# Kernel tuning notes

Hardware: AMD Instinct MI355X
Metric: run time of the kernel (lower is better)

The kernel has to match this reference:

```python
import jax, jax.numpy as jnp
from jax import lax
import numpy as np

H = 2048
LX = 32
LY = 32


def setup_inputs() -> dict:
    key = jax.random.key(0)
    ks = jax.random.split(key, 9)
    N = LX * LY
    s = 1.0 / np.sqrt(H).astype(np.float32)
    inp = {
        "x": jax.random.normal(ks[0], (N,), jnp.float32),
        # embed: Dense(1 -> H)
        "We": jax.random.normal(ks[1], (1, H), jnp.float32),
        "be": jnp.zeros((H,), jnp.float32),
        # GRUCell input gates (with bias)
        "Wir": jax.random.normal(ks[2], (H, H), jnp.float32) * s,
        "bir": jnp.zeros((H,), jnp.float32),
        "Wiz": jax.random.normal(ks[3], (H, H), jnp.float32) * s,
        "biz": jnp.zeros((H,), jnp.float32),
        "Win": jax.random.normal(ks[4], (H, H), jnp.float32) * s,
        "bin_": jnp.zeros((H,), jnp.float32),
        # GRUCell recurrent gates (hr/hz bias-free, hn with bias, as in flax)
        "Whr": jax.random.normal(ks[5], (H, H), jnp.float32) * s,
        "Whz": jax.random.normal(ks[6], (H, H), jnp.float32) * s,
        "Whn": jax.random.normal(ks[7], (H, H), jnp.float32) * s,
        "bhn": jnp.zeros((H,), jnp.float32),
        "Lx": LX,
        "Ly": LY,
    }
    return inp


def snake_order(Lx: int, Ly: int):
    idx = np.arange(Lx * Ly).reshape(Ly, Lx)
    idx[1::2] = idx[1::2, ::-1]  # reverse odd rows -> snake pattern
    return jnp.asarray(idx.reshape(-1))


def reference(x, We, be, Wir, bir, Wiz, biz, Win, bin_, Whr, Whz, Whn, bhn, Lx, Ly):
    order = snake_order(Lx, Ly)                      # (N,) visit order
    # embed each scalar site value: Dense(1->H), vectorized over all sites
    xe = x[order][:, None] * We[0][None, :] + be     # (N, H)
    # precompute input-gate projections for all steps (same math, batched)
    a_r = xe @ Wir + bir                             # (N, H)
    a_z = xe @ Wiz + biz
    a_n = xe @ Win + bin_
    h0 = jnp.zeros((Whr.shape[0],), xe.dtype)

    def step(h, g):
        ar, az, an = g
        r = jax.nn.sigmoid(ar + h @ Whr)
        z = jax.nn.sigmoid(az + h @ Whz)
        n = jnp.tanh(an + r * (h @ Whn + bhn))
        h_new = (1.0 - z) * n + z * h
        return h_new, None

    h, _ = lax.scan(step, h0, (a_r, a_z, a_n))
    return h
```

## Files before the change

kernel.cpp:

```cpp
#include <hip/hip_runtime.h>

#define HDIM 2048
#define TSTEPS 1024
#define NBLK 256
#define NTHR 512

typedef unsigned long long ull;

__device__ __forceinline__ int snake_src(int t) {
    int y = t >> 5, p = t & 31;
    return (y & 1) ? (y * 32 + 31 - p) : t;
}
__device__ __forceinline__ float sigmoid_f(float v) {
    return __builtin_amdgcn_rcpf(1.f + __expf(-v));
}
__device__ __forceinline__ float tanh_f(float v) {
    return 1.f - 2.f * __builtin_amdgcn_rcpf(__expf(2.f * v) + 1.f);
}

__global__ __launch_bounds__(NTHR, 2) void gru_all(
    const float* __restrict__ x,
    const float* __restrict__ We,  const float* __restrict__ be,
    const float* __restrict__ Wir, const float* __restrict__ bir,
    const float* __restrict__ Wiz, const float* __restrict__ biz,
    const float* __restrict__ Win, const float* __restrict__ bin_,
    const float* __restrict__ Whr, const float* __restrict__ Whz,
    const float* __restrict__ Whn, const float* __restrict__ bhn,
    float* __restrict__ out, ull* __restrict__ s0, ull* __restrict__ s1)
{
    const int tid  = threadIdx.x;
    const int blk  = blockIdx.x;
    const int c    = tid & 7;
    const int r    = tid >> 3;
    const int col  = blk * 8 + c;
    const int row0 = r * 32;
    const int lane = tid & 63, wv = tid >> 6;

    __shared__ __align__(16) float lds_h[2304];
    __shared__ float sBe[HDIM];
    __shared__ float red[8][6][8];

    for (int i = tid; i < HDIM; i += NTHR) { lds_h[i] = We[i]; sBe[i] = be[i]; }
    __syncthreads();

    float wr[32], wz[32], wn[32];
#pragma unroll
    for (int k = 0; k < 32; ++k) {
        size_t off = (size_t)(row0 + k) * HDIM + col;
        wr[k] = Whr[off];
        wz[k] = Whz[off];
        wn[k] = Whn[off];
    }

    float eR=0,eZ=0,eN=0,bRa=0,bZa=0,bNa=0;
#pragma unroll 8
    for (int k = 0; k < 32; ++k) {
        size_t off = (size_t)(row0 + k) * HDIM + col;
        float we = lds_h[row0 + k], bb = sBe[row0 + k];
        float w0 = Wir[off], w1 = Wiz[off], w2 = Win[off];
        eR  = fmaf(we, w0, eR);  bRa = fmaf(bb, w0, bRa);
        eZ  = fmaf(we, w1, eZ);  bZa = fmaf(bb, w1, bZa);
        eN  = fmaf(we, w2, eN);  bNa = fmaf(bb, w2, bNa);
    }
#pragma unroll
    for (int m = 8; m < 64; m <<= 1) {
        eR  += __shfl_xor(eR,  m, 64); eZ  += __shfl_xor(eZ,  m, 64);
        eN  += __shfl_xor(eN,  m, 64); bRa += __shfl_xor(bRa, m, 64);
        bZa += __shfl_xor(bZa, m, 64); bNa += __shfl_xor(bNa, m, 64);
    }
    if (lane < 8) {
        red[wv][0][lane]=eR;  red[wv][1][lane]=eZ;  red[wv][2][lane]=eN;
        red[wv][3][lane]=bRa; red[wv][4][lane]=bZa; red[wv][5][lane]=bNa;
    }
    __syncthreads();

    float vrc=0,vzc=0,vnc=0,crc=0,czc=0,cnc=0,bhc=0;
    if (tid < 8) {
#pragma unroll
        for (int w = 0; w < 8; ++w) {
            vrc += red[w][0][tid]; vzc += red[w][1][tid]; vnc += red[w][2][tid];
            crc += red[w][3][tid]; czc += red[w][4][tid]; cnc += red[w][5][tid];
        }
        crc += bir[col]; czc += biz[col]; cnc += bin_[col];
        bhc = bhn[col];

        float x0 = x[snake_src(0)];
        float ar = fmaf(x0, vrc, crc);
        float az = fmaf(x0, vzc, czc);
        float an = fmaf(x0, vnc, cnc);
        float rg = sigmoid_f(ar), zg = sigmoid_f(az);
        float ng = tanh_f(fmaf(rg, bhc, an));
        float h1 = (1.f - zg) * ng;
        ull pkt = (1ULL << 32) | (ull)__float_as_uint(h1);
        __hip_atomic_store(&s1[col], pkt, __ATOMIC_RELAXED, __HIP_MEMORY_SCOPE_AGENT);
    }

    const int sbase = tid * 4;
    const int lwb   = sbase + ((sbase >> 5) << 2);
    const int lrb   = row0  + ((row0  >> 5) << 2);

    for (int t = 1; t < TSTEPS; ++t) {
        ull* sin  = (t & 1) ? s1 : s0;
        ull* sout = (t & 1) ? s0 : s1;

        ull v0, v1, v2, v3;
        for (;;) {
            v0 = __hip_atomic_load(&sin[sbase+0], __ATOMIC_RELAXED, __HIP_MEMORY_SCOPE_AGENT);
            v1 = __hip_atomic_load(&sin[sbase+1], __ATOMIC_RELAXED, __HIP_MEMORY_SCOPE_AGENT);
            v2 = __hip_atomic_load(&sin[sbase+2], __ATOMIC_RELAXED, __HIP_MEMORY_SCOPE_AGENT);
            v3 = __hip_atomic_load(&sin[sbase+3], __ATOMIC_RELAXED, __HIP_MEMORY_SCOPE_AGENT);
            if ((int)(v0 >> 32) == t && (int)(v1 >> 32) == t &&
                (int)(v2 >> 32) == t && (int)(v3 >> 32) == t) break;
        }
        float4 hq = make_float4(__uint_as_float((unsigned)v0), __uint_as_float((unsigned)v1),
                                __uint_as_float((unsigned)v2), __uint_as_float((unsigned)v3));
        *(float4*)&lds_h[lwb] = hq;
        __syncthreads();

        float a0 = 0.f, a1 = 0.f, a2 = 0.f;
#pragma unroll
        for (int k = 0; k < 32; ++k) {
            float hv = lds_h[lrb + k];
            a0 = fmaf(hv, wr[k], a0);
            a1 = fmaf(hv, wz[k], a1);
            a2 = fmaf(hv, wn[k], a2);
        }
#pragma unroll
        for (int m = 8; m < 64; m <<= 1) {
            a0 += __shfl_xor(a0, m, 64);
            a1 += __shfl_xor(a1, m, 64);
            a2 += __shfl_xor(a2, m, 64);
        }
        if (lane < 8) { red[wv][0][lane]=a0; red[wv][1][lane]=a1; red[wv][2][lane]=a2; }
        __syncthreads();

        if (tid < 8) {
            float Sr=0, Sz=0, Sn=0;
#pragma unroll
            for (int w = 0; w < 8; ++w) {
                Sr += red[w][0][tid]; Sz += red[w][1][tid]; Sn += red[w][2][tid];
            }
            float xt = x[snake_src(t)];
            float ar = fmaf(xt, vrc, crc) + Sr;
            float az = fmaf(xt, vzc, czc) + Sz;
            float an = fmaf(xt, vnc, cnc);
            float rg = sigmoid_f(ar), zg = sigmoid_f(az);
            float ng = tanh_f(an + rg * (Sn + bhc));
            float hold = lds_h[col + ((col >> 5) << 2)];
            float hnew = (1.f - zg) * ng + zg * hold;
            if (t == TSTEPS - 1) {
                out[col] = hnew;
            } else {
                ull pkt = ((ull)(unsigned)(t + 1) << 32) | (ull)__float_as_uint(hnew);
                __hip_atomic_store(&sout[col], pkt, __ATOMIC_RELAXED, __HIP_MEMORY_SCOPE_AGENT);
            }
        }
        __syncthreads();
    }
}

extern "C" void kernel_launch(void* const* d_in, const int* in_sizes, int n_in,
                              void* d_out, int out_size, void* d_ws, size_t ws_size,
                              hipStream_t stream) {
    const float* x    = (const float*)d_in[0];
    const float* We   = (const float*)d_in[1];
    const float* be   = (const float*)d_in[2];
    const float* Wir  = (const float*)d_in[3];
    const float* bir  = (const float*)d_in[4];
    const float* Wiz  = (const float*)d_in[5];
    const float* biz  = (const float*)d_in[6];
    const float* Win  = (const float*)d_in[7];
    const float* bin_ = (const float*)d_in[8];
    const float* Whr  = (const float*)d_in[9];
    const float* Whz  = (const float*)d_in[10];
    const float* Whn  = (const float*)d_in[11];
    const float* bhn  = (const float*)d_in[12];

    ull* s0 = (ull*)d_ws;
    ull* s1 = s0 + HDIM;

    gru_all<<<NBLK, NTHR, 0, stream>>>(x, We, be, Wir, bir, Wiz, biz, Win, bin_,
                                       Whr, Whz, Whn, bhn,
                                       (float*)d_out, s0, s1);
}
```

Baseline: 2.678 ms.

## Map one column per wavefront to remove cross-wave reduction and barriers

Remaps threads so each wavefront owns one output column and each lane covers 32 rows. The full dot-product reduction becomes a wave-level shuffle, which removes the shared-memory reduction array and two of the three barriers per step. Double-buffers the hidden-state LDS array so one barrier per step suffices, and caches the snake-ordered x values in LDS. Weight loads now stride by row across lanes (less coalesced at setup), and every wave computes the gate math redundantly, with only lane 0 publishing the result.

```diff
diff --git a/kernel.cpp b/kernel.cpp
--- a/kernel.cpp
+++ b/kernel.cpp
@@ -17,6 +17,7 @@
 __device__ __forceinline__ float tanh_f(float v) {
     return 1.f - 2.f * __builtin_amdgcn_rcpf(__expf(2.f * v) + 1.f);
 }
+__device__ __forceinline__ int P(int i) { return i + (i >> 5); }
 
 __global__ __launch_bounds__(NTHR, 2) void gru_all(
     const float* __restrict__ x,
@@ -30,18 +31,15 @@
 {
     const int tid  = threadIdx.x;
     const int blk  = blockIdx.x;
-    const int c    = tid & 7;
-    const int r    = tid >> 3;
-    const int col  = blk * 8 + c;
-    const int row0 = r * 32;
-    const int lane = tid & 63, wv = tid >> 6;
+    const int lane = tid & 63;
+    const int wv   = tid >> 6;
+    const int col  = blk * 8 + wv;
+    const int row0 = lane * 32;
 
-    __shared__ __align__(16) float lds_h[2304];
-    __shared__ float sBe[HDIM];
-    __shared__ float red[8][6][8];
+    __shared__ float hbuf[2][2112];
+    __shared__ float xs_l[TSTEPS];
 
-    for (int i = tid; i < HDIM; i += NTHR) { lds_h[i] = We[i]; sBe[i] = be[i]; }
-    __syncthreads();
+    for (int i = tid; i < TSTEPS; i += NTHR) xs_l[i] = x[snake_src(i)];
 
     float wr[32], wz[32], wn[32];
 #pragma unroll
@@ -52,56 +50,50 @@
         wn[k] = Whn[off];
     }
 
-    float eR=0,eZ=0,eN=0,bRa=0,bZa=0,bNa=0;
+    float vrc = 0, vzc = 0, vnc = 0, crc = 0, czc = 0, cnc = 0;
 #pragma unroll 8
     for (int k = 0; k < 32; ++k) {
         size_t off = (size_t)(row0 + k) * HDIM + col;
-        float we = lds_h[row0 + k], bb = sBe[row0 + k];
+        float we = We[row0 + k], bb = be[row0 + k];
         float w0 = Wir[off], w1 = Wiz[off], w2 = Win[off];
-        eR  = fmaf(we, w0, eR);  bRa = fmaf(bb, w0, bRa);
-        eZ  = fmaf(we, w1, eZ);  bZa = fmaf(bb, w1, bZa);
-        eN  = fmaf(we, w2, eN);  bNa = fmaf(bb, w2, bNa);
+        vrc = fmaf(we, w0, vrc);  crc = fmaf(bb, w0, crc);
+        vzc = fmaf(we, w1, vzc);  czc = fmaf(bb, w1, czc);
+        vnc = fmaf(we, w2, vnc);  cnc = fmaf(bb, w2, cnc);
     }
 #pragma unroll
-    for (int m = 8; m < 64; m <<= 1) {
-        eR  += __shfl_xor(eR,  m, 64); eZ  += __shfl_xor(eZ,  m, 64);
-        eN  += __shfl_xor(eN,  m, 64); bRa += __shfl_xor(bRa, m, 64);
-        bZa += __shfl_xor(bZa, m, 64); bNa += __shfl_xor(bNa, m, 64);
+    for (int m = 1; m < 64; m <<= 1) {
+        vrc += __shfl_xor(vrc, m, 64); vzc += __shfl_xor(vzc, m, 64);
+        vnc += __shfl_xor(vnc, m, 64); crc += __shfl_xor(crc, m, 64);
+        czc += __shfl_xor(czc, m, 64); cnc += __shfl_xor(cnc, m, 64);
     }
-    if (lane < 8) {
-        red[wv][0][lane]=eR;  red[wv][1][lane]=eZ;  red[wv][2][lane]=eN;
-        red[wv][3][lane]=bRa; red[wv][4][lane]=bZa; red[wv][5][lane]=bNa;
-    }
+    crc += bir[col]; czc += biz[col]; cnc += bin_[col];
+    const float bhc = bhn[col];
+
     __syncthreads();
 
-    float vrc=0,vzc=0,vnc=0,crc=0,czc=0,cnc=0,bhc=0;
-    if (tid < 8) {
-#pragma unroll
-        for (int w = 0; w < 8; ++w) {
-            vrc += red[w][0][tid]; vzc += red[w][1][tid]; vnc += red[w][2][tid];
-            crc += red[w][3][tid]; czc += red[w][4][tid]; cnc += red[w][5][tid];
-        }
-        crc += bir[col]; czc += biz[col]; cnc += bin_[col];
-        bhc = bhn[col];
-
-        float x0 = x[snake_src(0)];
+    {
+        float x0 = xs_l[0];
         float ar = fmaf(x0, vrc, crc);
         float az = fmaf(x0, vzc, czc);
         float an = fmaf(x0, vnc, cnc);
         float rg = sigmoid_f(ar), zg = sigmoid_f(az);
         float ng = tanh_f(fmaf(rg, bhc, an));
         float h1 = (1.f - zg) * ng;
-        ull pkt = (1ULL << 32) | (ull)__float_as_uint(h1);
-        __hip_atomic_store(&s1[col], pkt, __ATOMIC_RELAXED, __HIP_MEMORY_SCOPE_AGENT);
+        if (lane == 0) {
+            ull pkt = (1ULL << 32) | (ull)__float_as_uint(h1);
+            __hip_atomic_store(&s1[col], pkt, __ATOMIC_RELAXED, __HIP_MEMORY_SCOPE_AGENT);
+        }
     }
 
     const int sbase = tid * 4;
-    const int lwb   = sbase + ((sbase >> 5) << 2);
-    const int lrb   = row0  + ((row0  >> 5) << 2);
+    const int pwb   = sbase + (sbase >> 5);
+    const int prb   = row0 + lane;
+    const int pcol  = P(col);
 
     for (int t = 1; t < TSTEPS; ++t) {
         ull* sin  = (t & 1) ? s1 : s0;
         ull* sout = (t & 1) ? s0 : s1;
+        float* hb = hbuf[t & 1];
 
         ull v0, v1, v2, v3;
         for (;;) {
@@ -112,42 +104,36 @@
             if ((int)(v0 >> 32) == t && (int)(v1 >> 32) == t &&
                 (int)(v2 >> 32) == t && (int)(v3 >> 32) == t) break;
         }
-        float4 hq = make_float4(__uint_as_float((unsigned)v0), __uint_as_float((unsigned)v1),
-                                __uint_as_float((unsigned)v2), __uint_as_float((unsigned)v3));
-        *(float4*)&lds_h[lwb] = hq;
+        hb[pwb + 0] = __uint_as_float((unsigned)v0);
+        hb[pwb + 1] = __uint_as_float((unsigned)v1);
+        hb[pwb + 2] = __uint_as_float((unsigned)v2);
+        hb[pwb + 3] = __uint_as_float((unsigned)v3);
         __syncthreads();
 
         float a0 = 0.f, a1 = 0.f, a2 = 0.f;
 #pragma unroll
         for (int k = 0; k < 32; ++k) {
-            float hv = lds_h[lrb + k];
+            float hv = hb[prb + k];
             a0 = fmaf(hv, wr[k], a0);
             a1 = fmaf(hv, wz[k], a1);
             a2 = fmaf(hv, wn[k], a2);
         }
 #pragma unroll
-        for (int m = 8; m < 64; m <<= 1) {
+        for (int m = 1; m < 64; m <<= 1) {
             a0 += __shfl_xor(a0, m, 64);
             a1 += __shfl_xor(a1, m, 64);
             a2 += __shfl_xor(a2, m, 64);
         }
-        if (lane < 8) { red[wv][0][lane]=a0; red[wv][1][lane]=a1; red[wv][2][lane]=a2; }
-        __syncthreads();
 
-        if (tid < 8) {
-            float Sr=0, Sz=0, Sn=0;
-#pragma unroll
-            for (int w = 0; w < 8; ++w) {
-                Sr += red[w][0][tid]; Sz += red[w][1][tid]; Sn += red[w][2][tid];
-            }
-            float xt = x[snake_src(t)];
-            float ar = fmaf(xt, vrc, crc) + Sr;
-            float az = fmaf(xt, vzc, czc) + Sz;
-            float an = fmaf(xt, vnc, cnc);
-            float rg = sigmoid_f(ar), zg = sigmoid_f(az);
-            float ng = tanh_f(an + rg * (Sn + bhc));
-            float hold = lds_h[col + ((col >> 5) << 2)];
-            float hnew = (1.f - zg) * ng + zg * hold;
+        float xt = xs_l[t];
+        float ar = fmaf(xt, vrc, crc) + a0;
+        float az = fmaf(xt, vzc, czc) + a1;
+        float an = fmaf(xt, vnc, cnc);
+        float rg = sigmoid_f(ar), zg = sigmoid_f(az);
+        float ng = tanh_f(an + rg * (a2 + bhc));
+        float hold = hb[pcol];
+        float hnew = (1.f - zg) * ng + zg * hold;
+        if (lane == 0) {
             if (t == TSTEPS - 1) {
                 out[col] = hnew;
             } else {
@@ -155,7 +141,6 @@
                 __hip_atomic_store(&sout[col], pkt, __ATOMIC_RELAXED, __HIP_MEMORY_SCOPE_AGENT);
             }
         }
-        __syncthreads();
     }
 }
 
```

After: 6.742 ms. 152% more time.
